# Kernel tuning notes

Measured on AMD Instinct MI355X. Metric: run time of the kernel, lower is better.

The kernel has to match this reference:

```python
import jax, jax.numpy as jnp
import numpy as np
import math

EMBED_DIM = 128
NUM_HEADS = 8
HDIM = EMBED_DIM // NUM_HEADS


def setup_inputs() -> dict:
    key = jax.random.key(0)
    kq, kh, km, k1, k2, k3, k4 = jax.random.split(key, 7)
    B, NQ, GS = 32, 1024, 1024
    q = jax.random.normal(kq, (B, NQ, EMBED_DIM), dtype=jnp.float32)
    h = jax.random.normal(kh, (B, GS, EMBED_DIM), dtype=jnp.float32)
    mask = jax.random.bernoulli(km, 0.15, (B, NQ, GS))
    stdv = 1.0 / math.sqrt(HDIM)
    Wq = jax.random.uniform(k1, (NUM_HEADS, EMBED_DIM, HDIM), jnp.float32, -stdv, stdv)
    Wk = jax.random.uniform(k2, (NUM_HEADS, EMBED_DIM, HDIM), jnp.float32, -stdv, stdv)
    Wv = jax.random.uniform(k3, (NUM_HEADS, EMBED_DIM, HDIM), jnp.float32, -stdv, stdv)
    stdv_o = 1.0 / math.sqrt(EMBED_DIM)
    Wout = jax.random.uniform(k4, (NUM_HEADS, HDIM, EMBED_DIM), jnp.float32, -stdv_o, stdv_o)
    return {"q": q, "h": h, "mask": mask, "Wq": Wq, "Wk": Wk, "Wv": Wv, "Wout": Wout}


def reference(q, h, mask, Wq, Wk, Wv, Wout):
    norm = 1.0 / math.sqrt(HDIM)
    # per-head projections: [h, b, n, e]
    Q = jnp.einsum('bnd,hde->hbne', q, Wq)
    K = jnp.einsum('bgd,hde->hbge', h, Wk)
    V = jnp.einsum('bgd,hde->hbge', h, Wv)
    compat = norm * jnp.einsum('hbne,hbge->hbng', Q, K)  # [h,b,nq,gs]
    m = mask[None]  # broadcast over heads
    compat = jnp.where(m, -jnp.inf, compat)
    attn = jax.nn.softmax(compat, axis=-1)
    attn = jnp.where(m, 0.0, attn)
    heads = jnp.einsum('hbng,hbge->hbne', attn, V)
    out = jnp.einsum('hbne,hed->bnd', heads, Wout)
    return out
```

## Files before the change

### kernel.cpp

```cpp
#include <hip/hip_runtime.h>

typedef unsigned short u16;
typedef unsigned int   u32;
typedef short bf16x8 __attribute__((ext_vector_type(8)));
typedef float f32x2  __attribute__((ext_vector_type(2)));
typedef float f32x4  __attribute__((ext_vector_type(4)));
typedef float f32x16 __attribute__((ext_vector_type(16)));

#define NB  32
#define NQ  1024
#define GS  1024
#define NH  8
#define SCQ (0.25f * 1.4426950408889634f)
#define MBIG (-1.0e30f)

#define MFMA16(a, b, c) __builtin_amdgcn_mfma_f32_16x16x32_bf16(a, b, c, 0, 0, 0)
#define MFMA32(a, b, c) __builtin_amdgcn_mfma_f32_32x32x16_bf16(a, b, c, 0, 0, 0)

__device__ __forceinline__ u16 f2bf(float f) {
    u32 u = __float_as_uint(f);
    return (u16)((u + 0x7fffu + ((u >> 16) & 1u)) >> 16);
}
__device__ __forceinline__ u32 pk2bf(float a, float b) {
    u32 ua = __float_as_uint(a) + 0x8000u;
    u32 ub = __float_as_uint(b) + 0x8000u;
    return __builtin_amdgcn_perm(ub, ua, 0x07060302u);
}

template <int MODE>
__device__ __forceinline__ void mgemm(const float* __restrict__ Ain,
                                      const float* __restrict__ Wraw,
                                      float wsc,
                                      u16* __restrict__ outb,
                                      u16* Ws, int row0) {
    const int t    = threadIdx.x;
    const int wv   = t >> 6;
    const int lane = t & 63;
    const int quad = lane >> 4;
    const int c    = lane & 15;

#pragma unroll
    for (int g0 = 0; g0 < 2048; g0 += 256) {
        int idx  = g0 + t;
        int hk   = idx >> 1, half = idx & 1;
        int k    = hk & 127;
        int col0 = (hk >> 7) * 16 + half * 8;
        const float4* wp = (const float4*)&Wraw[hk * 16 + half * 8];
        float4 w0 = wp[0], w1 = wp[1];
        Ws[(col0 + 0) * 136 + k] = f2bf(w0.x * wsc);
        Ws[(col0 + 1) * 136 + k] = f2bf(w0.y * wsc);
        Ws[(col0 + 2) * 136 + k] = f2bf(w0.z * wsc);
        Ws[(col0 + 3) * 136 + k] = f2bf(w0.w * wsc);
        Ws[(col0 + 4) * 136 + k] = f2bf(w1.x * wsc);
        Ws[(col0 + 5) * 136 + k] = f2bf(w1.y * wsc);
        Ws[(col0 + 6) * 136 + k] = f2bf(w1.z * wsc);
        Ws[(col0 + 7) * 136 + k] = f2bf(w1.w * wsc);
    }

    const float* a0p = &Ain[(size_t)(row0 + wv * 32 + c) * 128];
    const float* a1p = &Ain[(size_t)(row0 + wv * 32 + 16 + c) * 128];
    bf16x8 af0[4], af1[4];
#pragma unroll
    for (int kt = 0; kt < 4; ++kt) {
        int k0 = kt * 32 + quad * 8;
        float4 x0 = *(const float4*)&a0p[k0];
        float4 x1 = *(const float4*)&a0p[k0 + 4];
        float4 y0 = *(const float4*)&a1p[k0];
        float4 y1 = *(const float4*)&a1p[k0 + 4];
        int4 p0, p1;
        p0.x = (int)pk2bf(x0.x, x0.y);  p0.y = (int)pk2bf(x0.z, x0.w);
        p0.z = (int)pk2bf(x1.x, x1.y);  p0.w = (int)pk2bf(x1.z, x1.w);
        p1.x = (int)pk2bf(y0.x, y0.y);  p1.y = (int)pk2bf(y0.z, y0.w);
        p1.z = (int)pk2bf(y1.x, y1.y);  p1.w = (int)pk2bf(y1.z, y1.w);
        __builtin_memcpy(&af0[kt], &p0, 16);
        __builtin_memcpy(&af1[kt], &p1, 16);
    }
    __syncthreads();

    const f32x4 zf = {0.f, 0.f, 0.f, 0.f};
    f32x4 acc[2][8];
#pragma unroll
    for (int s = 0; s < 2; ++s)
#pragma unroll
        for (int j = 0; j < 8; ++j) acc[s][j] = zf;

#pragma unroll
    for (int kt = 0; kt < 4; ++kt) {
#pragma unroll
        for (int j = 0; j < 8; ++j) {
            bf16x8 bfr = *(const bf16x8*)&Ws[(j * 16 + c) * 136 + kt * 32 + quad * 8];
            acc[0][j] = MFMA16(af0[kt], bfr, acc[0][j]);
            acc[1][j] = MFMA16(af1[kt], bfr, acc[1][j]);
        }
    }

    __syncthreads();
    u16* Os = Ws;
#pragma unroll
    for (int s = 0; s < 2; ++s)
#pragma unroll
        for (int j = 0; j < 8; ++j)
#pragma unroll
            for (int r = 0; r < 4; ++r) {
                int lrow = wv * 32 + s * 16 + quad * 4 + r;
                int col  = j * 16 + c;
                u16 v = f2bf(acc[s][j][r]);
                if (MODE == 0) {
                    Os[lrow * 136 + col] = v;
                } else {
                    int u   = lrow & 15;
                    int sw  = ((u >> 2) ^ (u >> 3)) & 1;
                    int tbp = lrow ^ (sw ? 12 : 0);
                    Os[col * 136 + tbp] = v;
                }
            }
    __syncthreads();

    if (MODE == 0) {
#pragma unroll
        for (int it = 0; it < 8; ++it) {
            int chunk = it * 256 + t;
            int lrow = chunk >> 4, c0 = (chunk & 15) * 8;
            *(int4*)&outb[(size_t)(row0 + lrow) * 128 + c0] =
                *(const int4*)&Os[lrow * 136 + c0];
        }
    } else {
        int bI = row0 >> 10, tb0 = row0 & 1023;
#pragma unroll
        for (int it = 0; it < 8; ++it) {
            int chunk = it * 256 + t;
            int col = chunk >> 4, t0 = (chunk & 15) * 8;
            *(int4*)&outb[(size_t)bI * (128 * 1024) + (size_t)col * 1024 + tb0 + t0] =
                *(const int4*)&Os[col * 136 + t0];
        }
    }
}

__global__ __launch_bounds__(256, 3) void proj_mfma(const float* __restrict__ q,
                                                    const float* __restrict__ h,
                                                    const float* __restrict__ Wq,
                                                    const float* __restrict__ Wk,
                                                    const float* __restrict__ Wv,
                                                    const float* __restrict__ Wout,
                                                    u16* __restrict__ Qb,
                                                    u16* __restrict__ Kb,
                                                    u16* __restrict__ Vtg,
                                                    u16* __restrict__ Wob) {
    __shared__ u16 Ws[128 * 136];
    int y = blockIdx.y;
    if (y == 3) {
        if (blockIdx.x < 64) {
            int i = blockIdx.x * 256 + threadIdx.x;
            int d = i >> 7, he = i & 127;
            Wob[i] = f2bf(Wout[(he >> 4) * 2048 + (he & 15) * 128 + d]);
        }
        return;
    }
    int row0 = blockIdx.x * 128;
    if (y == 0)      mgemm<0>(q, Wq, SCQ,  Qb,  Ws, row0);
    else if (y == 1) mgemm<0>(h, Wk, 1.0f, Kb,  Ws, row0);
    else             mgemm<2>(h, Wv, 1.0f, Vtg, Ws, row0);
}

__global__ __launch_bounds__(512, 4) void flash_mfma(const u16* __restrict__ Qb,
                                                     const u16* __restrict__ Kb,
                                                     const u16* __restrict__ Vtg,
                                                     const int* __restrict__ mask,
                                                     const u16* __restrict__ Wob,
                                                     float* __restrict__ out) {
    __shared__ u16 Kt[64 * 136];
    __shared__ u16 Vtt[128 * 72];
    __shared__ float Mf[32 * 68];

    const int b    = blockIdx.x;
    const int q0   = blockIdx.y * 32;
    const int t    = threadIdx.x;
    const int hh   = t >> 6;
    const int lane = t & 63;
    const int quad = lane >> 4;
    const int c    = lane & 15;
    const int qq   = lane & 31;
    const int hi   = lane >> 5;

    bf16x8 qf = *(const bf16x8*)&Qb[((size_t)b * NQ + q0 + qq) * 128 +
                                    hh * 16 + hi * 8];

    f32x16 O32;
#pragma unroll
    for (int r = 0; r < 16; ++r) O32[r] = 0.f;
    float lsum = 0.f;

    const int skey = t >> 4;
    const int sd0  = (t & 15) * 8;
    const int vdim = t >> 2;
    const int vs0  = (t & 3) * 8;
    const int mrow = t >> 4;
    const int mk0  = (t & 15) * 2;

    const u16* Kptr = &Kb[((size_t)b * GS + skey) * 128 + sd0];
    const u16* Vptr = &Vtg[(size_t)b * (128 * 1024) + (size_t)vdim * 1024 + vs0];
    const int* Mptr = &mask[((size_t)b * NQ + q0 + mrow) * GS + mk0];

    int4 kreg0 = *(const int4*)Kptr;
    int4 kreg1 = *(const int4*)(Kptr + 32 * 128);
    int4 vreg0 = *(const int4*)Vptr;
    int4 vreg1 = *(const int4*)(Vptr + 32);
    int2 mreg0 = *(const int2*)Mptr;
    int2 mreg1 = *(const int2*)(Mptr + 32);

    for (int g0 = 0; g0 < GS; g0 += 64) {
        __syncthreads();
        *(int4*)&Kt[skey * 136 + sd0]        = kreg0;
        *(int4*)&Kt[(32 + skey) * 136 + sd0] = kreg1;
        *(int4*)&Vtt[vdim * 72 + vs0]        = vreg0;
        *(int4*)&Vtt[vdim * 72 + 32 + vs0]   = vreg1;
        f32x2 mm0, mm1;
        mm0.x = mreg0.x ? MBIG : 0.f;
        mm0.y = mreg0.y ? MBIG : 0.f;
        mm1.x = mreg1.x ? MBIG : 0.f;
        mm1.y = mreg1.y ? MBIG : 0.f;
        *(f32x2*)&Mf[mrow * 68 + mk0]      = mm0;
        *(f32x2*)&Mf[mrow * 68 + 32 + mk0] = mm1;
        __syncthreads();

        if (g0 + 64 < GS) {
            Kptr += 64 * 128;
            kreg0 = *(const int4*)Kptr;
            kreg1 = *(const int4*)(Kptr + 32 * 128);
            Vptr += 64;
            vreg0 = *(const int4*)Vptr;
            vreg1 = *(const int4*)(Vptr + 32);
            Mptr += 64;
            mreg0 = *(const int2*)Mptr;
            mreg1 = *(const int2*)(Mptr + 32);
        }

        bf16x8 kf0 = *(const bf16x8*)&Kt[qq * 136 + hh * 16 + hi * 8];
        bf16x8 kf1 = *(const bf16x8*)&Kt[(32 + qq) * 136 + hh * 16 + hi * 8];
        f32x16 c0, c1;
#pragma unroll
        for (int blk = 0; blk < 4; ++blk) {
            f32x4 m0 = *(const f32x4*)&Mf[qq * 68 + 8 * blk + 4 * hi];
            f32x4 m1 = *(const f32x4*)&Mf[qq * 68 + 32 + 8 * blk + 4 * hi];
            c0[4 * blk + 0] = m0.x;  c0[4 * blk + 1] = m0.y;
            c0[4 * blk + 2] = m0.z;  c0[4 * blk + 3] = m0.w;
            c1[4 * blk + 0] = m1.x;  c1[4 * blk + 1] = m1.y;
            c1[4 * blk + 2] = m1.z;  c1[4 * blk + 3] = m1.w;
        }
        f32x16 s0 = MFMA32(kf0, qf, c0);
        f32x16 s1 = MFMA32(kf1, qf, c1);

        bf16x8 vf0 = *(const bf16x8*)&Vtt[(hh * 16 + c) * 72 + hi * 8];
        bf16x8 vf1 = *(const bf16x8*)&Vtt[(hh * 16 + c) * 72 + 16 + hi * 8];
        bf16x8 vf2 = *(const bf16x8*)&Vtt[(hh * 16 + c) * 72 + 32 + hi * 8];
        bf16x8 vf3 = *(const bf16x8*)&Vtt[(hh * 16 + c) * 72 + 48 + hi * 8];

#pragma unroll
        for (int r = 0; r < 16; ++r) s0[r] = __builtin_amdgcn_exp2f(s0[r]);
        lsum += ((s0[0] + s0[1]) + (s0[2] + s0[3])) + ((s0[4] + s0[5]) + (s0[6] + s0[7])) +
                (((s0[8] + s0[9]) + (s0[10] + s0[11])) + ((s0[12] + s0[13]) + (s0[14] + s0[15])));
        {
            int4 pa, pb;
            pa.x = (int)pk2bf(s0[0],  s0[1]);  pa.y = (int)pk2bf(s0[2],  s0[3]);
            pa.z = (int)pk2bf(s0[4],  s0[5]);  pa.w = (int)pk2bf(s0[6],  s0[7]);
            pb.x = (int)pk2bf(s0[8],  s0[9]);  pb.y = (int)pk2bf(s0[10], s0[11]);
            pb.z = (int)pk2bf(s0[12], s0[13]); pb.w = (int)pk2bf(s0[14], s0[15]);
            bf16x8 p0, p1;
            __builtin_memcpy(&p0, &pa, 16);
            __builtin_memcpy(&p1, &pb, 16);
            O32 = MFMA32(vf0, p0, O32);
            O32 = MFMA32(vf1, p1, O32);
        }

#pragma unroll
        for (int r = 0; r < 16; ++r) s1[r] = __builtin_amdgcn_exp2f(s1[r]);
        lsum += ((s1[0] + s1[1]) + (s1[2] + s1[3])) + ((s1[4] + s1[5]) + (s1[6] + s1[7])) +
                (((s1[8] + s1[9]) + (s1[10] + s1[11])) + ((s1[12] + s1[13]) + (s1[14] + s1[15])));
        {
            int4 pa, pb;
            pa.x = (int)pk2bf(s1[0],  s1[1]);  pa.y = (int)pk2bf(s1[2],  s1[3]);
            pa.z = (int)pk2bf(s1[4],  s1[5]);  pa.w = (int)pk2bf(s1[6],  s1[7]);
            pb.x = (int)pk2bf(s1[8],  s1[9]);  pb.y = (int)pk2bf(s1[10], s1[11]);
            pb.z = (int)pk2bf(s1[12], s1[13]); pb.w = (int)pk2bf(s1[14], s1[15]);
            bf16x8 p2, p3;
            __builtin_memcpy(&p2, &pa, 16);
            __builtin_memcpy(&p3, &pb, 16);
            O32 = MFMA32(vf2, p2, O32);
            O32 = MFMA32(vf3, p3, O32);
        }
    }

    lsum += __shfl_xor(lsum, 32);
    float rl = (lsum > 0.f) ? 1.f / lsum : 0.f;

    u32 h0 = pk2bf(O32[0] * rl, O32[1] * rl);
    u32 h1 = pk2bf(O32[2] * rl, O32[3] * rl);
    u32 h2 = pk2bf(O32[4] * rl, O32[5] * rl);
    u32 h3 = pk2bf(O32[6] * rl, O32[7] * rl);
    __syncthreads();
    u16* Hs = Kt;
    int2 ha; ha.x = (int)h0; ha.y = (int)h1;
    int2 hb; hb.x = (int)h2; hb.y = (int)h3;
    *(int2*)&Hs[qq * 136 + hh * 16 + 4 * hi]     = ha;
    *(int2*)&Hs[qq * 136 + hh * 16 + 8 + 4 * hi] = hb;
    __syncthreads();

    const f32x4 zf = {0.f, 0.f, 0.f, 0.f};
    f32x4 oacc[2] = {zf, zf};
#pragma unroll
    for (int kt = 0; kt < 4; ++kt) {
        bf16x8 bfr = *(const bf16x8*)&Wob[(hh * 16 + c) * 128 + kt * 32 + quad * 8];
#pragma unroll
        for (int s = 0; s < 2; ++s) {
            bf16x8 af = *(const bf16x8*)&Hs[(s * 16 + c) * 136 + kt * 32 + quad * 8];
            oacc[s] = MFMA16(af, bfr, oacc[s]);
        }
    }
#pragma unroll
    for (int s = 0; s < 2; ++s)
#pragma unroll
        for (int r = 0; r < 4; ++r)
            out[((size_t)b * NQ + q0 + s * 16 + quad * 4 + r) * 128 + hh * 16 + c] =
                oacc[s][r];
}

extern "C" void kernel_launch(void* const* d_in, const int* in_sizes, int n_in,
                              void* d_out, int out_size, void* d_ws, size_t ws_size,
                              hipStream_t stream) {
    const float* q    = (const float*)d_in[0];
    const float* h    = (const float*)d_in[1];
    const int*   mask = (const int*)d_in[2];
    const float* Wq   = (const float*)d_in[3];
    const float* Wk   = (const float*)d_in[4];
    const float* Wv   = (const float*)d_in[5];
    const float* Wout = (const float*)d_in[6];
    float* out = (float*)d_out;

    const size_t NTOK = (size_t)NB * NQ;
    u16* Qb  = (u16*)d_ws;
    u16* Kb  = Qb + NTOK * 128;
    u16* Vtg = Kb + NTOK * 128;
    u16* Wob = Vtg + NTOK * 128;

    proj_mfma<<<dim3(256, 4), 256, 0, stream>>>(q, h, Wq, Wk, Wv, Wout,
                                                Qb, Kb, Vtg, Wob);
    flash_mfma<<<dim3(NB, NQ / 32), 512, 0, stream>>>(Qb, Kb, Vtg, mask,
                                                      Wob, out);
}
```

Baseline: 276.0 us.

## Process 64 queries per block to reuse staged K/V tiles twice

Each flash block now handles two 32-query groups instead of one, so every K and V tile staged into shared memory serves twice as many queries. This halves global K/V traffic and the number of sync rounds per query. In exchange each thread holds two output accumulators and two query fragments, which raises register pressure under launch_bounds(512,4), and the grid shrinks to half as many blocks.

```diff
diff --git a/kernel.cpp b/kernel.cpp
--- a/kernel.cpp
+++ b/kernel.cpp
@@ -170,10 +170,10 @@
                                                      float* __restrict__ out) {
     __shared__ u16 Kt[64 * 136];
     __shared__ u16 Vtt[128 * 72];
-    __shared__ float Mf[32 * 68];
+    __shared__ float Mf[64 * 68];
 
     const int b    = blockIdx.x;
-    const int q0   = blockIdx.y * 32;
+    const int q0   = blockIdx.y * 64;
     const int t    = threadIdx.x;
     const int hh   = t >> 6;
     const int lane = t & 63;
@@ -182,13 +182,18 @@
     const int qq   = lane & 31;
     const int hi   = lane >> 5;
 
-    bf16x8 qf = *(const bf16x8*)&Qb[((size_t)b * NQ + q0 + qq) * 128 +
+    bf16x8 qf[2];
+#pragma unroll
+    for (int g = 0; g < 2; ++g)
+        qf[g] = *(const bf16x8*)&Qb[((size_t)b * NQ + q0 + g * 32 + qq) * 128 +
                                     hh * 16 + hi * 8];
 
-    f32x16 O32;
-#pragma unroll
-    for (int r = 0; r < 16; ++r) O32[r] = 0.f;
-    float lsum = 0.f;
+    f32x16 O32[2];
+#pragma unroll
+    for (int g = 0; g < 2; ++g)
+#pragma unroll
+        for (int r = 0; r < 16; ++r) O32[g][r] = 0.f;
+    float lsum[2] = {0.f, 0.f};
 
     const int skey = t >> 4;
     const int sd0  = (t & 15) * 8;
@@ -199,14 +204,17 @@
 
     const u16* Kptr = &Kb[((size_t)b * GS + skey) * 128 + sd0];
     const u16* Vptr = &Vtg[(size_t)b * (128 * 1024) + (size_t)vdim * 1024 + vs0];
-    const int* Mptr = &mask[((size_t)b * NQ + q0 + mrow) * GS + mk0];
+    const int* Mptr0 = &mask[((size_t)b * NQ + q0 + mrow) * GS + mk0];
+    const int* Mptr1 = Mptr0 + (size_t)32 * GS;
 
     int4 kreg0 = *(const int4*)Kptr;
     int4 kreg1 = *(const int4*)(Kptr + 32 * 128);
     int4 vreg0 = *(const int4*)Vptr;
     int4 vreg1 = *(const int4*)(Vptr + 32);
-    int2 mreg0 = *(const int2*)Mptr;
-    int2 mreg1 = *(const int2*)(Mptr + 32);
+    int2 mreg0 = *(const int2*)Mptr0;
+    int2 mreg1 = *(const int2*)(Mptr0 + 32);
+    int2 mreg2 = *(const int2*)Mptr1;
+    int2 mreg3 = *(const int2*)(Mptr1 + 32);
 
     for (int g0 = 0; g0 < GS; g0 += 64) {
         __syncthreads();
@@ -214,13 +222,15 @@
         *(int4*)&Kt[(32 + skey) * 136 + sd0] = kreg1;
         *(int4*)&Vtt[vdim * 72 + vs0]        = vreg0;
         *(int4*)&Vtt[vdim * 72 + 32 + vs0]   = vreg1;
-        f32x2 mm0, mm1;
-        mm0.x = mreg0.x ? MBIG : 0.f;
-        mm0.y = mreg0.y ? MBIG : 0.f;
-        mm1.x = mreg1.x ? MBIG : 0.f;
-        mm1.y = mreg1.y ? MBIG : 0.f;
-        *(f32x2*)&Mf[mrow * 68 + mk0]      = mm0;
-        *(f32x2*)&Mf[mrow * 68 + 32 + mk0] = mm1;
+        f32x2 mm0, mm1, mm2, mm3;
+        mm0.x = mreg0.x ? MBIG : 0.f;  mm0.y = mreg0.y ? MBIG : 0.f;
+        mm1.x = mreg1.x ? MBIG : 0.f;  mm1.y = mreg1.y ? MBIG : 0.f;
+        mm2.x = mreg2.x ? MBIG : 0.f;  mm2.y = mreg2.y ? MBIG : 0.f;
+        mm3.x = mreg3.x ? MBIG : 0.f;  mm3.y = mreg3.y ? MBIG : 0.f;
+        *(f32x2*)&Mf[mrow * 68 + mk0]             = mm0;
+        *(f32x2*)&Mf[mrow * 68 + 32 + mk0]        = mm1;
+        *(f32x2*)&Mf[(32 + mrow) * 68 + mk0]      = mm2;
+        *(f32x2*)&Mf[(32 + mrow) * 68 + 32 + mk0] = mm3;
         __syncthreads();
 
         if (g0 + 64 < GS) {
@@ -230,94 +240,108 @@
             Vptr += 64;
             vreg0 = *(const int4*)Vptr;
             vreg1 = *(const int4*)(Vptr + 32);
-            Mptr += 64;
-            mreg0 = *(const int2*)Mptr;
-            mreg1 = *(const int2*)(Mptr + 32);
+            Mptr0 += 64;  Mptr1 += 64;
+            mreg0 = *(const int2*)Mptr0;
+            mreg1 = *(const int2*)(Mptr0 + 32);
+            mreg2 = *(const int2*)Mptr1;
+            mreg3 = *(const int2*)(Mptr1 + 32);
         }
 
         bf16x8 kf0 = *(const bf16x8*)&Kt[qq * 136 + hh * 16 + hi * 8];
         bf16x8 kf1 = *(const bf16x8*)&Kt[(32 + qq) * 136 + hh * 16 + hi * 8];
-        f32x16 c0, c1;
-#pragma unroll
-        for (int blk = 0; blk < 4; ++blk) {
-            f32x4 m0 = *(const f32x4*)&Mf[qq * 68 + 8 * blk + 4 * hi];
-            f32x4 m1 = *(const f32x4*)&Mf[qq * 68 + 32 + 8 * blk + 4 * hi];
-            c0[4 * blk + 0] = m0.x;  c0[4 * blk + 1] = m0.y;
-            c0[4 * blk + 2] = m0.z;  c0[4 * blk + 3] = m0.w;
-            c1[4 * blk + 0] = m1.x;  c1[4 * blk + 1] = m1.y;
-            c1[4 * blk + 2] = m1.z;  c1[4 * blk + 3] = m1.w;
-        }
-        f32x16 s0 = MFMA32(kf0, qf, c0);
-        f32x16 s1 = MFMA32(kf1, qf, c1);
-
         bf16x8 vf0 = *(const bf16x8*)&Vtt[(hh * 16 + c) * 72 + hi * 8];
         bf16x8 vf1 = *(const bf16x8*)&Vtt[(hh * 16 + c) * 72 + 16 + hi * 8];
         bf16x8 vf2 = *(const bf16x8*)&Vtt[(hh * 16 + c) * 72 + 32 + hi * 8];
         bf16x8 vf3 = *(const bf16x8*)&Vtt[(hh * 16 + c) * 72 + 48 + hi * 8];
 
 #pragma unroll
-        for (int r = 0; r < 16; ++r) s0[r] = __builtin_amdgcn_exp2f(s0[r]);
-        lsum += ((s0[0] + s0[1]) + (s0[2] + s0[3])) + ((s0[4] + s0[5]) + (s0[6] + s0[7])) +
-                (((s0[8] + s0[9]) + (s0[10] + s0[11])) + ((s0[12] + s0[13]) + (s0[14] + s0[15])));
-        {
-            int4 pa, pb;
-            pa.x = (int)pk2bf(s0[0],  s0[1]);  pa.y = (int)pk2bf(s0[2],  s0[3]);
-            pa.z = (int)pk2bf(s0[4],  s0[5]);  pa.w = (int)pk2bf(s0[6],  s0[7]);
-            pb.x = (int)pk2bf(s0[8],  s0[9]);  pb.y = (int)pk2bf(s0[10], s0[11]);
-            pb.z = (int)pk2bf(s0[12], s0[13]); pb.w = (int)pk2bf(s0[14], s0[15]);
-            bf16x8 p0, p1;
-            __builtin_memcpy(&p0, &pa, 16);
-            __builtin_memcpy(&p1, &pb, 16);
-            O32 = MFMA32(vf0, p0, O32);
-            O32 = MFMA32(vf1, p1, O32);
-        }
-
-#pragma unroll
-        for (int r = 0; r < 16; ++r) s1[r] = __builtin_amdgcn_exp2f(s1[r]);
-        lsum += ((s1[0] + s1[1]) + (s1[2] + s1[3])) + ((s1[4] + s1[5]) + (s1[6] + s1[7])) +
-                (((s1[8] + s1[9]) + (s1[10] + s1[11])) + ((s1[12] + s1[13]) + (s1[14] + s1[15])));
-        {
-            int4 pa, pb;
-            pa.x = (int)pk2bf(s1[0],  s1[1]);  pa.y = (int)pk2bf(s1[2],  s1[3]);
-            pa.z = (int)pk2bf(s1[4],  s1[5]);  pa.w = (int)pk2bf(s1[6],  s1[7]);
-            pb.x = (int)pk2bf(s1[8],  s1[9]);  pb.y = (int)pk2bf(s1[10], s1[11]);
-            pb.z = (int)pk2bf(s1[12], s1[13]); pb.w = (int)pk2bf(s1[14], s1[15]);
-            bf16x8 p2, p3;
-            __builtin_memcpy(&p2, &pa, 16);
-            __builtin_memcpy(&p3, &pb, 16);
-            O32 = MFMA32(vf2, p2, O32);
-            O32 = MFMA32(vf3, p3, O32);
-        }
-    }
-
-    lsum += __shfl_xor(lsum, 32);
-    float rl = (lsum > 0.f) ? 1.f / lsum : 0.f;
-
-    u32 h0 = pk2bf(O32[0] * rl, O32[1] * rl);
-    u32 h1 = pk2bf(O32[2] * rl, O32[3] * rl);
-    u32 h2 = pk2bf(O32[4] * rl, O32[5] * rl);
-    u32 h3 = pk2bf(O32[6] * rl, O32[7] * rl);
+        for (int g = 0; g < 2; ++g) {
+            const float* mf = &Mf[(g * 32 + qq) * 68];
+            {
+                f32x16 c0;
+#pragma unroll
+                for (int blk = 0; blk < 4; ++blk) {
+                    f32x4 m0 = *(const f32x4*)&mf[8 * blk + 4 * hi];
+                    c0[4 * blk + 0] = m0.x;  c0[4 * blk + 1] = m0.y;
+                    c0[4 * blk + 2] = m0.z;  c0[4 * blk + 3] = m0.w;
+                }
+                f32x16 s0 = MFMA32(kf0, qf[g], c0);
+#pragma unroll
+                for (int r = 0; r < 16; ++r) s0[r] = __builtin_amdgcn_exp2f(s0[r]);
+                lsum[g] += ((s0[0] + s0[1]) + (s0[2] + s0[3])) +
+                           ((s0[4] + s0[5]) + (s0[6] + s0[7])) +
+                           (((s0[8] + s0[9]) + (s0[10] + s0[11])) +
+                            ((s0[12] + s0[13]) + (s0[14] + s0[15])));
+                int4 pa, pb;
+                pa.x = (int)pk2bf(s0[0],  s0[1]);  pa.y = (int)pk2bf(s0[2],  s0[3]);
+                pa.z = (int)pk2bf(s0[4],  s0[5]);  pa.w = (int)pk2bf(s0[6],  s0[7]);
+                pb.x = (int)pk2bf(s0[8],  s0[9]);  pb.y = (int)pk2bf(s0[10], s0[11]);
+                pb.z = (int)pk2bf(s0[12], s0[13]); pb.w = (int)pk2bf(s0[14], s0[15]);
+                bf16x8 p0, p1;
+                __builtin_memcpy(&p0, &pa, 16);
+                __builtin_memcpy(&p1, &pb, 16);
+                O32[g] = MFMA32(vf0, p0, O32[g]);
+                O32[g] = MFMA32(vf1, p1, O32[g]);
+            }
+            {
+                f32x16 c1;
+#pragma unroll
+                for (int blk = 0; blk < 4; ++blk) {
+                    f32x4 m1 = *(const f32x4*)&mf[32 + 8 * blk + 4 * hi];
+                    c1[4 * blk + 0] = m1.x;  c1[4 * blk + 1] = m1.y;
+                    c1[4 * blk + 2] = m1.z;  c1[4 * blk + 3] = m1.w;
+                }
+                f32x16 s1 = MFMA32(kf1, qf[g], c1);
+#pragma unroll
+                for (int r = 0; r < 16; ++r) s1[r] = __builtin_amdgcn_exp2f(s1[r]);
+                lsum[g] += ((s1[0] + s1[1]) + (s1[2] + s1[3])) +
+                           ((s1[4] + s1[5]) + (s1[6] + s1[7])) +
+                           (((s1[8] + s1[9]) + (s1[10] + s1[11])) +
+                            ((s1[12] + s1[13]) + (s1[14] + s1[15])));
+                int4 pa, pb;
+                pa.x = (int)pk2bf(s1[0],  s1[1]);  pa.y = (int)pk2bf(s1[2],  s1[3]);
+                pa.z = (int)pk2bf(s1[4],  s1[5]);  pa.w = (int)pk2bf(s1[6],  s1[7]);
+                pb.x = (int)pk2bf(s1[8],  s1[9]);  pb.y = (int)pk2bf(s1[10], s1[11]);
+                pb.z = (int)pk2bf(s1[12], s1[13]); pb.w = (int)pk2bf(s1[14], s1[15]);
+                bf16x8 p2, p3;
+                __builtin_memcpy(&p2, &pa, 16);
+                __builtin_memcpy(&p3, &pb, 16);
+                O32[g] = MFMA32(vf2, p2, O32[g]);
+                O32[g] = MFMA32(vf3, p3, O32[g]);
+            }
+        }
+    }
+
     __syncthreads();
     u16* Hs = Kt;
-    int2 ha; ha.x = (int)h0; ha.y = (int)h1;
-    int2 hb; hb.x = (int)h2; hb.y = (int)h3;
-    *(int2*)&Hs[qq * 136 + hh * 16 + 4 * hi]     = ha;
-    *(int2*)&Hs[qq * 136 + hh * 16 + 8 + 4 * hi] = hb;
+#pragma unroll
+    for (int g = 0; g < 2; ++g) {
+        float l = lsum[g] + __shfl_xor(lsum[g], 32);
+        float rl = (l > 0.f) ? 1.f / l : 0.f;
+        u32 h0 = pk2bf(O32[g][0] * rl, O32[g][1] * rl);
+        u32 h1 = pk2bf(O32[g][2] * rl, O32[g][3] * rl);
+        u32 h2 = pk2bf(O32[g][4] * rl, O32[g][5] * rl);
+        u32 h3 = pk2bf(O32[g][6] * rl, O32[g][7] * rl);
+        int2 ha; ha.x = (int)h0; ha.y = (int)h1;
+        int2 hb; hb.x = (int)h2; hb.y = (int)h3;
+        *(int2*)&Hs[(g * 32 + qq) * 136 + hh * 16 + 4 * hi]     = ha;
+        *(int2*)&Hs[(g * 32 + qq) * 136 + hh * 16 + 8 + 4 * hi] = hb;
+    }
     __syncthreads();
 
     const f32x4 zf = {0.f, 0.f, 0.f, 0.f};
-    f32x4 oacc[2] = {zf, zf};
+    f32x4 oacc[4] = {zf, zf, zf, zf};
 #pragma unroll
     for (int kt = 0; kt < 4; ++kt) {
         bf16x8 bfr = *(const bf16x8*)&Wob[(hh * 16 + c) * 128 + kt * 32 + quad * 8];
 #pragma unroll
-        for (int s = 0; s < 2; ++s) {
+        for (int s = 0; s < 4; ++s) {
             bf16x8 af = *(const bf16x8*)&Hs[(s * 16 + c) * 136 + kt * 32 + quad * 8];
             oacc[s] = MFMA16(af, bfr, oacc[s]);
         }
     }
 #pragma unroll
-    for (int s = 0; s < 2; ++s)
+    for (int s = 0; s < 4; ++s)
 #pragma unroll
         for (int r = 0; r < 4; ++r)
             out[((size_t)b * NQ + q0 + s * 16 + quad * 4 + r) * 128 + hh * 16 + c] =
@@ -344,6 +368,6 @@
 
     proj_mfma<<<dim3(256, 4), 256, 0, stream>>>(q, h, Wq, Wk, Wv, Wout,
                                                 Qb, Kb, Vtg, Wob);
-    flash_mfma<<<dim3(NB, NQ / 32), 512, 0, stream>>>(Qb, Kb, Vtg, mask,
+    flash_mfma<<<dim3(NB, NQ / 64), 512, 0, stream>>>(Qb, Kb, Vtg, mask,
                                                       Wob, out);
 }
```

After: 490.6 us. 1.78x slower.

## Process 64 query rows per block with 1024 threads to share K/V tiles

Applied to the files above, without the earlier changes.

Each flash-attention block now covers 64 queries instead of 32, using 16 waves (8 heads × 2 query groups) that share each staged K and V tile in shared memory. This halves the global K/V traffic per query and spreads the staging loads over more threads, so each thread issues one vector load per operand. In exchange blocks are larger (1024 threads) with fewer blocks in the grid, and the mask staging tile doubles in size. The launch bound now asks for 8 blocks per CU, which may not be achievable given register and LDS use.

```diff
diff --git a/kernel.cpp b/kernel.cpp
--- a/kernel.cpp
+++ b/kernel.cpp
@@ -162,27 +162,30 @@
     else             mgemm<2>(h, Wv, 1.0f, Vtg, Ws, row0);
 }
 
-__global__ __launch_bounds__(512, 4) void flash_mfma(const u16* __restrict__ Qb,
-                                                     const u16* __restrict__ Kb,
-                                                     const u16* __restrict__ Vtg,
-                                                     const int* __restrict__ mask,
-                                                     const u16* __restrict__ Wob,
-                                                     float* __restrict__ out) {
+__global__ __launch_bounds__(1024, 8) void flash_mfma(const u16* __restrict__ Qb,
+                                                      const u16* __restrict__ Kb,
+                                                      const u16* __restrict__ Vtg,
+                                                      const int* __restrict__ mask,
+                                                      const u16* __restrict__ Wob,
+                                                      float* __restrict__ out) {
     __shared__ u16 Kt[64 * 136];
     __shared__ u16 Vtt[128 * 72];
-    __shared__ float Mf[32 * 68];
+    __shared__ float Mf[64 * 68];
 
     const int b    = blockIdx.x;
-    const int q0   = blockIdx.y * 32;
+    const int q0   = blockIdx.y * 64;
     const int t    = threadIdx.x;
-    const int hh   = t >> 6;
+    const int wave = t >> 6;
+    const int hh   = wave & 7;
+    const int qg   = wave >> 3;
     const int lane = t & 63;
     const int quad = lane >> 4;
     const int c    = lane & 15;
     const int qq   = lane & 31;
     const int hi   = lane >> 5;
-
-    bf16x8 qf = *(const bf16x8*)&Qb[((size_t)b * NQ + q0 + qq) * 128 +
+    const int qrow = qg * 32 + qq;
+
+    bf16x8 qf = *(const bf16x8*)&Qb[((size_t)b * NQ + q0 + qrow) * 128 +
                                     hh * 16 + hi * 8];
 
     f32x16 O32;
@@ -192,47 +195,35 @@
 
     const int skey = t >> 4;
     const int sd0  = (t & 15) * 8;
-    const int vdim = t >> 2;
-    const int vs0  = (t & 3) * 8;
+    const int vdim = t >> 3;
+    const int vs0  = (t & 7) * 8;
     const int mrow = t >> 4;
-    const int mk0  = (t & 15) * 2;
+    const int mk0  = (t & 15) * 4;
 
     const u16* Kptr = &Kb[((size_t)b * GS + skey) * 128 + sd0];
     const u16* Vptr = &Vtg[(size_t)b * (128 * 1024) + (size_t)vdim * 1024 + vs0];
     const int* Mptr = &mask[((size_t)b * NQ + q0 + mrow) * GS + mk0];
 
-    int4 kreg0 = *(const int4*)Kptr;
-    int4 kreg1 = *(const int4*)(Kptr + 32 * 128);
-    int4 vreg0 = *(const int4*)Vptr;
-    int4 vreg1 = *(const int4*)(Vptr + 32);
-    int2 mreg0 = *(const int2*)Mptr;
-    int2 mreg1 = *(const int2*)(Mptr + 32);
+    int4 kreg = *(const int4*)Kptr;
+    int4 vreg = *(const int4*)Vptr;
+    int4 mreg = *(const int4*)Mptr;
 
     for (int g0 = 0; g0 < GS; g0 += 64) {
         __syncthreads();
-        *(int4*)&Kt[skey * 136 + sd0]        = kreg0;
-        *(int4*)&Kt[(32 + skey) * 136 + sd0] = kreg1;
-        *(int4*)&Vtt[vdim * 72 + vs0]        = vreg0;
-        *(int4*)&Vtt[vdim * 72 + 32 + vs0]   = vreg1;
-        f32x2 mm0, mm1;
-        mm0.x = mreg0.x ? MBIG : 0.f;
-        mm0.y = mreg0.y ? MBIG : 0.f;
-        mm1.x = mreg1.x ? MBIG : 0.f;
-        mm1.y = mreg1.y ? MBIG : 0.f;
-        *(f32x2*)&Mf[mrow * 68 + mk0]      = mm0;
-        *(f32x2*)&Mf[mrow * 68 + 32 + mk0] = mm1;
+        *(int4*)&Kt[skey * 136 + sd0] = kreg;
+        *(int4*)&Vtt[vdim * 72 + vs0] = vreg;
+        f32x4 mm;
+        mm.x = mreg.x ? MBIG : 0.f;
+        mm.y = mreg.y ? MBIG : 0.f;
+        mm.z = mreg.z ? MBIG : 0.f;
+        mm.w = mreg.w ? MBIG : 0.f;
+        *(f32x4*)&Mf[mrow * 68 + mk0] = mm;
         __syncthreads();
 
         if (g0 + 64 < GS) {
-            Kptr += 64 * 128;
-            kreg0 = *(const int4*)Kptr;
-            kreg1 = *(const int4*)(Kptr + 32 * 128);
-            Vptr += 64;
-            vreg0 = *(const int4*)Vptr;
-            vreg1 = *(const int4*)(Vptr + 32);
-            Mptr += 64;
-            mreg0 = *(const int2*)Mptr;
-            mreg1 = *(const int2*)(Mptr + 32);
+            Kptr += 64 * 128;  kreg = *(const int4*)Kptr;
+            Vptr += 64;        vreg = *(const int4*)Vptr;
+            Mptr += 64;        mreg = *(const int4*)Mptr;
         }
 
         bf16x8 kf0 = *(const bf16x8*)&Kt[qq * 136 + hh * 16 + hi * 8];
@@ -240,8 +231,8 @@
         f32x16 c0, c1;
 #pragma unroll
         for (int blk = 0; blk < 4; ++blk) {
-            f32x4 m0 = *(const f32x4*)&Mf[qq * 68 + 8 * blk + 4 * hi];
-            f32x4 m1 = *(const f32x4*)&Mf[qq * 68 + 32 + 8 * blk + 4 * hi];
+            f32x4 m0 = *(const f32x4*)&Mf[qrow * 68 + 8 * blk + 4 * hi];
+            f32x4 m1 = *(const f32x4*)&Mf[qrow * 68 + 32 + 8 * blk + 4 * hi];
             c0[4 * blk + 0] = m0.x;  c0[4 * blk + 1] = m0.y;
             c0[4 * blk + 2] = m0.z;  c0[4 * blk + 3] = m0.w;
             c1[4 * blk + 0] = m1.x;  c1[4 * blk + 1] = m1.y;
@@ -301,8 +292,8 @@
     u16* Hs = Kt;
     int2 ha; ha.x = (int)h0; ha.y = (int)h1;
     int2 hb; hb.x = (int)h2; hb.y = (int)h3;
-    *(int2*)&Hs[qq * 136 + hh * 16 + 4 * hi]     = ha;
-    *(int2*)&Hs[qq * 136 + hh * 16 + 8 + 4 * hi] = hb;
+    *(int2*)&Hs[qrow * 136 + hh * 16 + 4 * hi]     = ha;
+    *(int2*)&Hs[qrow * 136 + hh * 16 + 8 + 4 * hi] = hb;
     __syncthreads();
 
     const f32x4 zf = {0.f, 0.f, 0.f, 0.f};
@@ -312,7 +303,8 @@
         bf16x8 bfr = *(const bf16x8*)&Wob[(hh * 16 + c) * 128 + kt * 32 + quad * 8];
 #pragma unroll
         for (int s = 0; s < 2; ++s) {
-            bf16x8 af = *(const bf16x8*)&Hs[(s * 16 + c) * 136 + kt * 32 + quad * 8];
+            bf16x8 af = *(const bf16x8*)&Hs[(qg * 32 + s * 16 + c) * 136 +
+                                            kt * 32 + quad * 8];
             oacc[s] = MFMA16(af, bfr, oacc[s]);
         }
     }
@@ -320,8 +312,8 @@
     for (int s = 0; s < 2; ++s)
 #pragma unroll
         for (int r = 0; r < 4; ++r)
-            out[((size_t)b * NQ + q0 + s * 16 + quad * 4 + r) * 128 + hh * 16 + c] =
-                oacc[s][r];
+            out[((size_t)b * NQ + q0 + qg * 32 + s * 16 + quad * 4 + r) * 128 +
+                hh * 16 + c] = oacc[s][r];
 }
 
 extern "C" void kernel_launch(void* const* d_in, const int* in_sizes, int n_in,
@@ -344,6 +336,6 @@
 
     proj_mfma<<<dim3(256, 4), 256, 0, stream>>>(q, h, Wq, Wk, Wv, Wout,
                                                 Qb, Kb, Vtg, Wob);
-    flash_mfma<<<dim3(NB, NQ / 32), 512, 0, stream>>>(Qb, Kb, Vtg, mask,
-                                                      Wob, out);
-}
+    flash_mfma<<<dim3(NB, NQ / 64), 1024, 0, stream>>>(Qb, Kb, Vtg, mask,
+                                                       Wob, out);
+}
```

Result: slower. 589.6 us (+113.6%).
